# Optimization experiments

Hardware: AMD Instinct MI355X
Metric: run time of the kernel (lower is better)

The kernel has to match this reference:

```python
import jax, jax.numpy as jnp
from jax import lax
import numpy as np

NB = 4      # num_blocks
C = 1024    # model_channels
H = 16      # num_heads
P = 2       # patch_size
OUT_C = 64  # FinalLayer out_channels


def _sincos_1d(d, pos):
    omega = np.arange(d // 2, dtype=np.float64) / (d / 2.0)
    omega = 1.0 / 10000 ** omega
    out = np.einsum('m,d->md', pos.reshape(-1), omega)
    return np.concatenate([np.sin(out), np.cos(out)], axis=1)


def _sincos_2d(embed_dim, h, w):
    gh = np.arange(h, dtype=np.float32)
    gw = np.arange(w, dtype=np.float32)
    grid = np.stack(np.meshgrid(gw, gh), axis=0).reshape(2, 1, h, w)
    emb = np.concatenate([_sincos_1d(embed_dim // 2, grid[0]),
                          _sincos_1d(embed_dim // 2, grid[1])], axis=1)
    return jnp.asarray(emb, dtype=jnp.float32)  # (h*w, embed_dim)


def _ln(x, g, b, eps):
    mu = jnp.mean(x, axis=-1, keepdims=True)
    var = jnp.mean(jnp.square(x - mu), axis=-1, keepdims=True)
    y = (x - mu) * lax.rsqrt(var + eps)
    if g is not None:
        y = y * g + b
    return y


def _conv3x3(x, w, b):
    y = lax.conv_general_dilated(x, w, (1, 1), [(1, 1), (1, 1)],
                                 dimension_numbers=('NCHW', 'OIHW', 'NCHW'))
    return y + b[None, :, None, None]


def _forward(x, qkv_w, qkv_b, proj_w, proj_b, nq_g, nq_b, nk_g, nk_b,
             n1_g, n1_b, n2_g, n2_b, fc1_w, fc1_b, fc2_w, fc2_b,
             fin_w, fin_b, c1_w, c1_b, c2_w, c2_b):
    bs, l, c = x.shape
    h = w = int(np.sqrt(l))
    d = c // H
    scale = 1.0 / np.sqrt(d)
    x = x + _sincos_2d(c, h, w)[None]  # add 2D sincos pos embed
    for i in range(NB):
        # --- QK-norm attention ---
        res = x
        hn = _ln(x, n1_g[i], n1_b[i], 1e-5)
        qkv = hn @ qkv_w[i] + qkv_b[i]                 # (bs, l, 3c)
        q, k, v = jnp.split(qkv, 3, axis=-1)
        to_heads = lambda t: t.reshape(bs, l, H, d).transpose(0, 2, 1, 3)  # bhnd
        q = _ln(to_heads(q), nq_g[i], nq_b[i], 1e-5)
        k = _ln(to_heads(k), nk_g[i], nk_b[i], 1e-5)
        v = to_heads(v)
        attn = jax.nn.softmax(jnp.einsum('bhnd,bhmd->bhnm', q, k) * scale, axis=-1)
        o = jnp.einsum('bhnm,bhmd->bhnd', attn, v)
        o = o.transpose(0, 2, 1, 3).reshape(bs, l, c)
        x = res + (o @ proj_w[i] + proj_b[i])
        # --- MLP ---
        hn2 = _ln(x, n2_g[i], n2_b[i], 1e-5)
        mlp = jax.nn.gelu(hn2 @ fc1_w[i] + fc1_b[i], approximate=False) @ fc2_w[i] + fc2_b[i]
        x = x + mlp
    # --- final layer ---
    xf = _ln(x, None, None, 1e-6)
    xf = xf @ fin_w + fin_b                            # (bs, l, P*P*OUT_C)
    # --- unpatchify: last dim is flattened (c, p, p) ---
    xf = xf.reshape(bs, h, w, OUT_C, P, P)
    xf = jnp.einsum('bhwcpq->bhpwqc', xf).reshape(bs, h * P, w * P, OUT_C)
    xf = xf.transpose(0, 3, 1, 2)                      # (bs, 64, 64, 64)
    y = jax.nn.relu(_conv3x3(xf, c1_w, c1_b))
    y = _conv3x3(y, c2_w, c2_b)
    return y


def setup_inputs() -> dict:
    key = jax.random.key(0)
    ks = jax.random.split(key, 12)
    s = 0.02
    f = jnp.float32
    inp = {
        'x': jax.random.normal(ks[0], (2, 1024, C), f),
        'qkv_w': s * jax.random.normal(ks[1], (NB, C, 3 * C), f),
        'qkv_b': jnp.zeros((NB, 3 * C), f),
        'proj_w': s * jax.random.normal(ks[2], (NB, C, C), f),
        'proj_b': jnp.zeros((NB, C), f),
        'nq_g': jnp.ones((NB, C // H), f),
        'nq_b': jnp.zeros((NB, C // H), f),
        'nk_g': jnp.ones((NB, C // H), f),
        'nk_b': jnp.zeros((NB, C // H), f),
        'n1_g': jnp.ones((NB, C), f),
        'n1_b': jnp.zeros((NB, C), f),
        'n2_g': jnp.ones((NB, C), f),
        'n2_b': jnp.zeros((NB, C), f),
        'fc1_w': s * jax.random.normal(ks[3], (NB, C, 4 * C), f),
        'fc1_b': jnp.zeros((NB, 4 * C), f),
        'fc2_w': s * jax.random.normal(ks[4], (NB, 4 * C, C), f),
        'fc2_b': jnp.zeros((NB, C), f),
        'fin_w': s * jax.random.normal(ks[5], (C, P * P * OUT_C), f),
        'fin_b': jnp.zeros((P * P * OUT_C,), f),
        'c1_w': s * jax.random.normal(ks[6], (16, OUT_C, 3, 3), f),
        'c1_b': jnp.zeros((16,), f),
        'c2_w': s * jax.random.normal(ks[7], (3, 16, 3, 3), f),
        'c2_b': jnp.zeros((3,), f),
    }
    return inp


def reference(x, qkv_w, qkv_b, proj_w, proj_b, nq_g, nq_b, nk_g, nk_b,
              n1_g, n1_b, n2_g, n2_b, fc1_w, fc1_b, fc2_w, fc2_b,
              fin_w, fin_b, c1_w, c1_b, c2_w, c2_b):
    return _forward(x, qkv_w, qkv_b, proj_w, proj_b, nq_g, nq_b, nk_g, nk_b,
                    n1_g, n1_b, n2_g, n2_b, fc1_w, fc1_b, fc2_w, fc2_b,
                    fin_w, fin_b, c1_w, c1_b, c2_w, c2_b)
```

## Files before the change

### kernel.cpp

```cpp
#include <hip/hip_runtime.h>
#include <hip/hip_bf16.h>
#include <math.h>

typedef float floatx4 __attribute__((ext_vector_type(4)));
typedef short bf16x8 __attribute__((ext_vector_type(8)));

__device__ __forceinline__ unsigned short f2bf(float x) {
    union { float f; unsigned int u; } v; v.f = x;
    unsigned int r = v.u + 0x7fffu + ((v.u >> 16) & 1u);
    return (unsigned short)(r >> 16);
}

__device__ __forceinline__ void load_lds16(const void* g, void* l) {
    __builtin_amdgcn_global_load_lds(
        (const __attribute__((address_space(1))) unsigned int*)(uintptr_t)g,
        (__attribute__((address_space(3))) unsigned int*)(uintptr_t)l, 16, 0, 0);
}

__global__ void posembed_kernel(const float* __restrict__ xin, float* __restrict__ xb) {
    int idx = blockIdx.x * 256 + threadIdx.x;
    int c = idx & 1023;
    int n = (idx >> 10) & 1023;
    int pos = (c < 512) ? (n & 31) : (n >> 5);
    int cc = c & 511;
    int k = cc & 255;
    double om = exp(-(double)k * (9.210340371976184 / 256.0));
    double arg = (double)pos * om;
    float e = (float)((cc < 256) ? sin(arg) : cos(arg));
    xb[idx] = xin[idx] + e;
}

__global__ __launch_bounds__(256) void ln_kernel(const float* __restrict__ X,
                                                 unsigned short* __restrict__ Y,
                                                 const float* __restrict__ g,
                                                 const float* __restrict__ b,
                                                 float eps, int affine) {
    int row = blockIdx.x;
    const float4* xr = (const float4*)(X + (size_t)row * 1024);
    float4 x = xr[threadIdx.x];
    float s = x.x + x.y + x.z + x.w;
    float sq = x.x * x.x + x.y * x.y + x.z * x.z + x.w * x.w;
    __shared__ float red[8];
    #pragma unroll
    for (int off = 32; off; off >>= 1) { s += __shfl_xor(s, off); sq += __shfl_xor(sq, off); }
    int wid = threadIdx.x >> 6, lane = threadIdx.x & 63;
    if (!lane) { red[wid] = s; red[wid + 4] = sq; }
    __syncthreads();
    s = red[0] + red[1] + red[2] + red[3];
    sq = red[4] + red[5] + red[6] + red[7];
    float mu = s * (1.f / 1024.f);
    float var = sq * (1.f / 1024.f) - mu * mu;
    float rs = rsqrtf(var + eps);
    int c = threadIdx.x * 4;
    float4 y;
    if (affine) {
        y.x = (x.x - mu) * rs * g[c + 0] + b[c + 0];
        y.y = (x.y - mu) * rs * g[c + 1] + b[c + 1];
        y.z = (x.z - mu) * rs * g[c + 2] + b[c + 2];
        y.w = (x.w - mu) * rs * g[c + 3] + b[c + 3];
    } else {
        y.x = (x.x - mu) * rs; y.y = (x.y - mu) * rs;
        y.z = (x.z - mu) * rs; y.w = (x.w - mu) * rs;
    }
    ushort4 o;
    o.x = f2bf(y.x); o.y = f2bf(y.y); o.z = f2bf(y.z); o.w = f2bf(y.w);
    *(ushort4*)(Y + (size_t)row * 1024 + c) = o;
}

__global__ __launch_bounds__(256) void qkvprep_kernel(const float* __restrict__ qkv,
                                                      const float* __restrict__ nqg,
                                                      const float* __restrict__ nqb,
                                                      const float* __restrict__ nkg,
                                                      const float* __restrict__ nkb,
                                                      unsigned short* __restrict__ Qb,
                                                      unsigned short* __restrict__ Kb,
                                                      unsigned short* __restrict__ Vt) {
    __shared__ float t[64][65];
    int tid = threadIdx.x;
    int l0 = blockIdx.x * 64, h = blockIdx.y, b = blockIdx.z;
    for (int i = tid; i < 4096; i += 256) {
        int lr = i >> 6, dd = i & 63;
        t[lr][dd] = qkv[((size_t)(b * 1024 + l0 + lr)) * 3072 + 2048 + h * 64 + dd];
    }
    __syncthreads();
    for (int i = tid; i < 4096; i += 256) {
        int dd = i >> 6, lc = i & 63;
        Vt[((size_t)((b * 16 + h) * 64 + dd)) * 1024 + l0 + lc] = f2bf(t[lc][dd]);
    }
    int wave = tid >> 6, lane = tid & 63;
    float gq = nqg[lane], bq = nqb[lane], gk = nkg[lane], bk = nkb[lane];
    for (int i = 0; i < 16; i++) {
        int l = l0 + wave + 4 * i;
        const float* base = qkv + (size_t)(b * 1024 + l) * 3072 + h * 64 + lane;
        #pragma unroll
        for (int part = 0; part < 2; part++) {
            float v = base[part * 1024];
            float s = v, sq = v * v;
            #pragma unroll
            for (int off = 32; off; off >>= 1) { s += __shfl_xor(s, off); sq += __shfl_xor(sq, off); }
            float mu = s * (1.f / 64.f);
            float var = sq * (1.f / 64.f) - mu * mu;
            float rs = rsqrtf(var + 1e-5f);
            float y = (v - mu) * rs * (part ? gk : gq) + (part ? bk : bq);
            unsigned short* dst = part ? Kb : Qb;
            dst[(size_t)(b * 1024 + l) * 1024 + h * 64 + lane] = f2bf(y * (part ? 1.f : 0.125f));
        }
    }
}

__global__ __launch_bounds__(256) void attn_mfma(const unsigned short* __restrict__ Qb,
                                                 const unsigned short* __restrict__ Kb,
                                                 const unsigned short* __restrict__ Vt,
                                                 unsigned short* __restrict__ ob) {
    __shared__ short Ks[64 * 64];
    __shared__ short Vs[64 * 64];
    __shared__ short Pl[4][16 * 72];
    int tid = threadIdx.x;
    int lane = tid & 63, wave = tid >> 6;
    int ln16 = lane & 15, q = lane >> 4;
    int b = blockIdx.z, h = blockIdx.y, q0 = blockIdx.x * 64;
    int sw = ln16 & 7;
    int rc0 = (q ^ sw) * 8;
    int rc1 = ((4 + q) ^ sw) * 8;

    const unsigned short* qrow = Qb + ((size_t)(b * 1024 + q0 + wave * 16 + ln16)) * 1024 + h * 64;
    bf16x8 qf0 = *(const bf16x8*)(qrow + q * 8);
    bf16x8 qf1 = *(const bf16x8*)(qrow + 32 + q * 8);

    floatx4 o[4];
    #pragma unroll
    for (int td = 0; td < 4; td++) o[td] = (floatx4){0.f, 0.f, 0.f, 0.f};
    float mrow[4] = {-1e30f, -1e30f, -1e30f, -1e30f};
    float lrow[4] = {0.f, 0.f, 0.f, 0.f};

    const unsigned short* kbase0 = Kb + ((size_t)(b * 1024)) * 1024 + h * 64;
    const unsigned short* vbase0 = Vt + ((size_t)((b * 16 + h) * 64)) * 1024;

    for (int ch = 0; ch < 16; ch++) {
        int l0 = ch * 64;
        __syncthreads();
        #pragma unroll
        for (int it = 0; it < 2; it++) {
            int j = tid + it * 256;
            int row = j >> 3, g = j & 7, gc = g ^ (row & 7);
            load_lds16(kbase0 + (size_t)(l0 + row) * 1024 + gc * 8, &Ks[j * 8]);
            load_lds16(vbase0 + (size_t)row * 1024 + l0 + gc * 8, &Vs[j * 8]);
        }
        __syncthreads();

        floatx4 s[4];
        #pragma unroll
        for (int t = 0; t < 4; t++) {
            s[t] = (floatx4){0.f, 0.f, 0.f, 0.f};
            int kr = (t * 16 + ln16) * 64;
            bf16x8 kf0 = *(const bf16x8*)&Ks[kr + rc0];
            bf16x8 kf1 = *(const bf16x8*)&Ks[kr + rc1];
            s[t] = __builtin_amdgcn_mfma_f32_16x16x32_bf16(qf0, kf0, s[t], 0, 0, 0);
            s[t] = __builtin_amdgcn_mfma_f32_16x16x32_bf16(qf1, kf1, s[t], 0, 0, 0);
        }
        float cm[4], rs[4], p[4][4];
        #pragma unroll
        for (int r = 0; r < 4; r++)
            cm[r] = fmaxf(fmaxf(s[0][r], s[1][r]), fmaxf(s[2][r], s[3][r]));
        #pragma unroll
        for (int off = 1; off < 16; off <<= 1) {
            #pragma unroll
            for (int r = 0; r < 4; r++) cm[r] = fmaxf(cm[r], __shfl_xor(cm[r], off));
        }
        #pragma unroll
        for (int r = 0; r < 4; r++) {
            float mnew = fmaxf(mrow[r], cm[r]);
            float alpha = __expf(mrow[r] - mnew);
            mrow[r] = mnew;
            rs[r] = 0.f;
            #pragma unroll
            for (int t = 0; t < 4; t++) {
                p[t][r] = __expf(s[t][r] - mnew);
                rs[r] += p[t][r];
            }
            lrow[r] *= alpha;
            #pragma unroll
            for (int td = 0; td < 4; td++) o[td][r] *= alpha;
        }
        #pragma unroll
        for (int off = 1; off < 16; off <<= 1) {
            #pragma unroll
            for (int r = 0; r < 4; r++) rs[r] += __shfl_xor(rs[r], off);
        }
        #pragma unroll
        for (int r = 0; r < 4; r++) lrow[r] += rs[r];

        short* pw = &Pl[wave][0];
        #pragma unroll
        for (int t = 0; t < 4; t++)
            #pragma unroll
            for (int r = 0; r < 4; r++)
                pw[(q * 4 + r) * 72 + t * 16 + ln16] = (short)f2bf(p[t][r]);
        bf16x8 pf0 = *(const bf16x8*)&pw[ln16 * 72 + q * 8];
        bf16x8 pf1 = *(const bf16x8*)&pw[ln16 * 72 + 32 + q * 8];
        #pragma unroll
        for (int td = 0; td < 4; td++) {
            int vr = (td * 16 + ln16) * 64;
            bf16x8 vf0 = *(const bf16x8*)&Vs[vr + rc0];
            bf16x8 vf1 = *(const bf16x8*)&Vs[vr + rc1];
            o[td] = __builtin_amdgcn_mfma_f32_16x16x32_bf16(pf0, vf0, o[td], 0, 0, 0);
            o[td] = __builtin_amdgcn_mfma_f32_16x16x32_bf16(pf1, vf1, o[td], 0, 0, 0);
        }
    }
    #pragma unroll
    for (int td = 0; td < 4; td++) {
        #pragma unroll
        for (int r = 0; r < 4; r++) {
            int row = q0 + wave * 16 + q * 4 + r;
            int col = h * 64 + td * 16 + ln16;
            ob[((size_t)(b * 1024 + row)) * 1024 + col] = f2bf(o[td][r] / lrow[r]);
        }
    }
}

__global__ __launch_bounds__(256) void wtrans_kernel(const float* __restrict__ in,
                                                     unsigned short* __restrict__ out,
                                                     int K, int N) {
    __shared__ float t[64][65];
    int n0 = blockIdx.x * 64, k0 = blockIdx.y * 64, z = blockIdx.z;
    in  += (size_t)z * K * N;
    out += (size_t)z * N * K;
    for (int i = threadIdx.x; i < 4096; i += 256) {
        int kr = i >> 6, nc = i & 63;
        t[kr][nc] = in[(size_t)(k0 + kr) * N + n0 + nc];
    }
    __syncthreads();
    for (int i = threadIdx.x; i < 4096; i += 256) {
        int nr = i >> 6, kc = i & 63;
        out[(size_t)(n0 + nr) * K + k0 + kc] = f2bf(t[kc][nr]);
    }
}

template <int BM, int BN, int WM, int WN, int ACT, bool ADDC, bool OUTBF16, bool SPLITK>
__global__ __launch_bounds__(256) void gemm_bf16(const unsigned short* __restrict__ A,
                                                 const unsigned short* __restrict__ Bt,
                                                 const float* __restrict__ bias,
                                                 float* __restrict__ Cf,
                                                 unsigned short* __restrict__ Cb,
                                                 int M, int N, int K, int lda) {
    constexpr int MT = BM / (WM * 16);
    constexpr int NT = BN / (WN * 16);
    __shared__ short As[BM * 64];
    __shared__ short Bs[BN * 64];
    int tid = threadIdx.x;
    int lane = tid & 63, wave = tid >> 6;
    int wm = wave / WN, wn = wave % WN;
    int ln16 = lane & 15, q = lane >> 4;
    int m0 = blockIdx.y * BM, n0 = blockIdx.x * BN;
    int kOff = SPLITK ? blockIdx.z * K : 0;

    floatx4 acc[MT][NT];
    #pragma unroll
    for (int i = 0; i < MT; i++)
        #pragma unroll
        for (int j = 0; j < NT; j++) acc[i][j] = (floatx4){0.f, 0.f, 0.f, 0.f};

    int kSteps = K >> 6;
    for (int ks = 0; ks < kSteps; ks++) {
        int k0 = kOff + (ks << 6);
        #pragma unroll
        for (int it = 0; it < BM / 32; it++) {
            int i = tid + it * 256;
            int row = i >> 3, gc = (i & 7) ^ (row & 7);
            load_lds16(A + (size_t)(m0 + row) * lda + k0 + gc * 8, &As[i * 8]);
        }
        #pragma unroll
        for (int it = 0; it < BN / 32; it++) {
            int i = tid + it * 256;
            int row = i >> 3, gc = (i & 7) ^ (row & 7);
            load_lds16(Bt + (size_t)(n0 + row) * lda + k0 + gc * 8, &Bs[i * 8]);
        }
        __syncthreads();
        bf16x8 af[2][MT], bf[2][NT];
        #pragma unroll
        for (int h = 0; h < 2; h++) {
            #pragma unroll
            for (int mi = 0; mi < MT; mi++) {
                int row = wm * (BM / WM) + mi * 16 + ln16;
                af[h][mi] = *(const bf16x8*)&As[row * 64 + (((h * 4 + q) ^ (row & 7)) * 8)];
            }
            #pragma unroll
            for (int ni = 0; ni < NT; ni++) {
                int row = wn * (BN / WN) + ni * 16 + ln16;
                bf[h][ni] = *(const bf16x8*)&Bs[row * 64 + (((h * 4 + q) ^ (row & 7)) * 8)];
            }
        }
        #pragma unroll
        for (int h = 0; h < 2; h++)
            #pragma unroll
            for (int mi = 0; mi < MT; mi++)
                #pragma unroll
                for (int ni = 0; ni < NT; ni++)
                    acc[mi][ni] = __builtin_amdgcn_mfma_f32_16x16x32_bf16(af[h][mi], bf[h][ni], acc[mi][ni], 0, 0, 0);
        __syncthreads();
    }

    int q4 = q * 4;
    float* Cp = SPLITK ? (Cf + (size_t)blockIdx.z * M * N) : Cf;
    #pragma unroll
    for (int ni = 0; ni < NT; ni++) {
        int col = n0 + wn * (BN / WN) + ni * 16 + ln16;
        float bv = SPLITK ? 0.f : bias[col];
        #pragma unroll
        for (int mi = 0; mi < MT; mi++) {
            #pragma unroll
            for (int r = 0; r < 4; r++) {
                int row = m0 + wm * (BM / WM) + mi * 16 + q4 + r;
                size_t off = (size_t)row * N + col;
                float v = acc[mi][ni][r] + bv;
                if (!SPLITK && ACT == 1) v = 0.5f * v * (1.f + erff(v * 0.70710678118654752f));
                if (!SPLITK && ADDC) v += Cf[off];
                if (!SPLITK && OUTBF16) Cb[off] = f2bf(v);
                else Cp[off] = v;
            }
        }
    }
}

__global__ __launch_bounds__(256) void skreduce_kernel(const float* __restrict__ P,
                                                       const float* __restrict__ bias,
                                                       float* __restrict__ xb) {
    int idx = blockIdx.x * 256 + threadIdx.x;
    float4 a = ((const float4*)P)[idx];
    float4 b = ((const float4*)P)[idx + 524288];
    float4 x = ((float4*)xb)[idx];
    const float4 bb = *(const float4*)(bias + (idx & 255) * 4);
    x.x += a.x + b.x + bb.x;
    x.y += a.y + b.y + bb.y;
    x.z += a.z + b.z + bb.z;
    x.w += a.w + b.w + bb.w;
    ((float4*)xb)[idx] = x;
}

__global__ void unpatchify_kernel(const float* __restrict__ xf, float* __restrict__ img) {
    int idx = blockIdx.x * 256 + threadIdx.x;
    int x = idx & 63, y = (idx >> 6) & 63, ch = (idx >> 12) & 63, b = idx >> 18;
    int hh = y >> 1, ww = x >> 1, p = y & 1, qq = x & 1;
    img[idx] = xf[((size_t)b * 1024 + hh * 32 + ww) * 256 + ch * 4 + p * 2 + qq];
}

__global__ __launch_bounds__(256) void conv1_kernel(const float* __restrict__ img,
                                                    const float* __restrict__ w,
                                                    const float* __restrict__ bias,
                                                    float* __restrict__ out) {
    __shared__ float Ls[64 * 3 * 66];
    __shared__ float Ws[16 * 580];
    int tid = threadIdx.x;
    int y = blockIdx.x, b = blockIdx.y;
    for (int i = tid; i < 9216; i += 256) {
        int oc = i / 576, rem = i % 576;
        Ws[oc * 580 + rem] = w[i];
    }
    for (int i = tid; i < 12288; i += 256) {
        int r = i >> 6, x = i & 63;
        int ic = r / 3, ky = r % 3;
        int yy = y + ky - 1;
        float v = (yy >= 0 && yy < 64) ? img[((size_t)(b * 64 + ic) * 64 + yy) * 64 + x] : 0.f;
        Ls[(ic * 3 + ky) * 66 + x + 1] = v;
        if (x == 0)  Ls[(ic * 3 + ky) * 66 + 0]  = 0.f;
        if (x == 63) Ls[(ic * 3 + ky) * 66 + 65] = 0.f;
    }
    __syncthreads();
    int oc = tid >> 4, xg = (tid & 15) * 4;
    float bv = bias[oc];
    float acc0 = bv, acc1 = bv, acc2 = bv, acc3 = bv;
    for (int ic = 0; ic < 64; ic++) {
        const float* wr = &Ws[oc * 580 + ic * 9];
        float w00 = wr[0], w01 = wr[1], w02 = wr[2];
        float w10 = wr[3], w11 = wr[4], w12 = wr[5];
        float w20 = wr[6], w21 = wr[7], w22 = wr[8];
        const float* l0 = &Ls[(ic * 3 + 0) * 66 + xg];
        const float* l1 = &Ls[(ic * 3 + 1) * 66 + xg];
        const float* l2 = &Ls[(ic * 3 + 2) * 66 + xg];
        float a0 = l0[0], a1 = l0[1], a2 = l0[2], a3 = l0[3], a4 = l0[4], a5 = l0[5];
        float b0 = l1[0], b1 = l1[1], b2 = l1[2], b3 = l1[3], b4 = l1[4], b5 = l1[5];
        float c0 = l2[0], c1 = l2[1], c2 = l2[2], c3 = l2[3], c4 = l2[4], c5 = l2[5];
        acc0 += a0*w00 + a1*w01 + a2*w02 + b0*w10 + b1*w11 + b2*w12 + c0*w20 + c1*w21 + c2*w22;
        acc1 += a1*w00 + a2*w01 + a3*w02 + b1*w10 + b2*w11 + b3*w12 + c1*w20 + c2*w21 + c3*w22;
        acc2 += a2*w00 + a3*w01 + a4*w02 + b2*w10 + b3*w11 + b4*w12 + c2*w20 + c3*w21 + c4*w22;
        acc3 += a3*w00 + a4*w01 + a5*w02 + b3*w10 + b4*w11 + b5*w12 + c3*w20 + c4*w21 + c5*w22;
    }
    float* op = out + (((size_t)(b * 16 + oc) * 64 + y) * 64 + xg);
    op[0] = fmaxf(acc0, 0.f);
    op[1] = fmaxf(acc1, 0.f);
    op[2] = fmaxf(acc2, 0.f);
    op[3] = fmaxf(acc3, 0.f);
}

__global__ __launch_bounds__(256) void conv2_kernel(const float* __restrict__ in,
                                                    const float* __restrict__ w,
                                                    const float* __restrict__ bias,
                                                    float* __restrict__ out) {
    __shared__ float Ls[16 * 3 * 66];
    __shared__ float Ws[3 * 160];
    int tid = threadIdx.x;
    int y = blockIdx.x, b = blockIdx.y;
    for (int i = tid; i < 432; i += 256) {
        int oc = i / 144, rem = i % 144;
        Ws[oc * 160 + rem] = w[i];
    }
    for (int i = tid; i < 3072; i += 256) {
        int r = i >> 6, x = i & 63;
        int ic = r / 3, ky = r % 3;
        int yy = y + ky - 1;
        float v = (yy >= 0 && yy < 64) ? in[((size_t)(b * 16 + ic) * 64 + yy) * 64 + x] : 0.f;
        Ls[(ic * 3 + ky) * 66 + x + 1] = v;
        if (x == 0)  Ls[(ic * 3 + ky) * 66 + 0]  = 0.f;
        if (x == 63) Ls[(ic * 3 + ky) * 66 + 65] = 0.f;
    }
    __syncthreads();
    int oc = tid >> 6, x = tid & 63;
    if (oc < 3) {
        float acc = bias[oc];
        for (int ic = 0; ic < 16; ic++) {
            const float* wr = &Ws[oc * 160 + ic * 9];
            const float* l0 = &Ls[(ic * 3 + 0) * 66 + x];
            const float* l1 = &Ls[(ic * 3 + 1) * 66 + x];
            const float* l2 = &Ls[(ic * 3 + 2) * 66 + x];
            acc += l0[0]*wr[0] + l0[1]*wr[1] + l0[2]*wr[2]
                 + l1[0]*wr[3] + l1[1]*wr[4] + l1[2]*wr[5]
                 + l2[0]*wr[6] + l2[1]*wr[7] + l2[2]*wr[8];
        }
        out[((size_t)(b * 3 + oc) * 64 + y) * 64 + x] = acc;
    }
}

extern "C" void kernel_launch(void* const* d_in, const int* in_sizes, int n_in,
                              void* d_out, int out_size, void* d_ws, size_t ws_size,
                              hipStream_t stream) {
    const float* x_in   = (const float*)d_in[0];
    const float* qkv_w  = (const float*)d_in[1];
    const float* qkv_b  = (const float*)d_in[2];
    const float* proj_w = (const float*)d_in[3];
    const float* proj_b = (const float*)d_in[4];
    const float* nq_g   = (const float*)d_in[5];
    const float* nq_b   = (const float*)d_in[6];
    const float* nk_g   = (const float*)d_in[7];
    const float* nk_b   = (const float*)d_in[8];
    const float* n1_g   = (const float*)d_in[9];
    const float* n1_b   = (const float*)d_in[10];
    const float* n2_g   = (const float*)d_in[11];
    const float* n2_b   = (const float*)d_in[12];
    const float* fc1_w  = (const float*)d_in[13];
    const float* fc1_b  = (const float*)d_in[14];
    const float* fc2_w  = (const float*)d_in[15];
    const float* fc2_b  = (const float*)d_in[16];
    const float* fin_w  = (const float*)d_in[17];
    const float* fin_b  = (const float*)d_in[18];
    const float* c1_w   = (const float*)d_in[19];
    const float* c1_b   = (const float*)d_in[20];
    const float* c2_w   = (const float*)d_in[21];
    const float* c2_b   = (const float*)d_in[22];
    float* out = (float*)d_out;

    char* w = (char*)d_ws;
    float* xb           = (float*)w;          w += (size_t)2 * 1024 * 1024 * 4;
    unsigned short* hnb = (unsigned short*)w; w += (size_t)2 * 1024 * 1024 * 2;
    float* qkv          = (float*)w;          w += (size_t)2 * 1024 * 3072 * 4;
    unsigned short* obb = (unsigned short*)w; w += (size_t)2 * 1024 * 1024 * 2;
    unsigned short* mhb = (unsigned short*)w; w += (size_t)2 * 1024 * 4096 * 2;
    float* xf           = (float*)w;          w += (size_t)2 * 1024 * 256 * 4;
    float* img          = (float*)w;          w += (size_t)2 * 64 * 64 * 64 * 4;
    float* c1o          = (float*)w;          w += (size_t)2 * 16 * 64 * 64 * 4;
    unsigned short* Qb  = (unsigned short*)w; w += (size_t)2 * 1024 * 1024 * 2;
    unsigned short* Kb  = (unsigned short*)w; w += (size_t)2 * 1024 * 1024 * 2;
    unsigned short* Vt  = (unsigned short*)w; w += (size_t)2 * 16 * 64 * 1024 * 2;
    float* skb          = (float*)w;          w += (size_t)2 * 2048 * 1024 * 4;
    unsigned short* WQ  = (unsigned short*)w; w += (size_t)4 * 1024 * 3072 * 2;
    unsigned short* WP  = (unsigned short*)w; w += (size_t)4 * 1024 * 1024 * 2;
    unsigned short* W1  = (unsigned short*)w; w += (size_t)4 * 1024 * 4096 * 2;
    unsigned short* W2  = (unsigned short*)w; w += (size_t)4 * 4096 * 1024 * 2;
    unsigned short* WF  = (unsigned short*)w; w += (size_t)1024 * 256 * 2;

    wtrans_kernel<<<dim3(48, 16, 4), 256, 0, stream>>>(qkv_w, WQ, 1024, 3072);
    wtrans_kernel<<<dim3(16, 16, 4), 256, 0, stream>>>(proj_w, WP, 1024, 1024);
    wtrans_kernel<<<dim3(64, 16, 4), 256, 0, stream>>>(fc1_w, W1, 1024, 4096);
    wtrans_kernel<<<dim3(16, 64, 4), 256, 0, stream>>>(fc2_w, W2, 4096, 1024);
    wtrans_kernel<<<dim3(4, 16, 1), 256, 0, stream>>>(fin_w, WF, 1024, 256);

    posembed_kernel<<<8192, 256, 0, stream>>>(x_in, xb);

    for (int i = 0; i < 4; i++) {
        ln_kernel<<<2048, 256, 0, stream>>>(xb, hnb, n1_g + i * 1024, n1_b + i * 1024, 1e-5f, 1);
        gemm_bf16<64, 128, 2, 2, 0, false, false, false><<<dim3(24, 32), 256, 0, stream>>>(
            hnb, WQ + (size_t)i * 3072 * 1024, qkv_b + i * 3072, qkv, nullptr, 2048, 3072, 1024, 1024);
        qkvprep_kernel<<<dim3(16, 16, 2), 256, 0, stream>>>(
            qkv, nq_g + i * 64, nq_b + i * 64, nk_g + i * 64, nk_b + i * 64, Qb, Kb, Vt);
        attn_mfma<<<dim3(16, 16, 2), 256, 0, stream>>>(Qb, Kb, Vt, obb);
        gemm_bf16<64, 64, 2, 2, 0, true, false, false><<<dim3(16, 32), 256, 0, stream>>>(
            obb, WP + (size_t)i * 1024 * 1024, proj_b + i * 1024, xb, nullptr, 2048, 1024, 1024, 1024);
        ln_kernel<<<2048, 256, 0, stream>>>(xb, hnb, n2_g + i * 1024, n2_b + i * 1024, 1e-5f, 1);
        gemm_bf16<64, 128, 2, 2, 1, false, true, false><<<dim3(32, 32), 256, 0, stream>>>(
            hnb, W1 + (size_t)i * 4096 * 1024, fc1_b + i * 4096, nullptr, mhb, 2048, 4096, 1024, 1024);
        gemm_bf16<64, 64, 2, 2, 0, false, false, true><<<dim3(16, 32, 2), 256, 0, stream>>>(
            mhb, W2 + (size_t)i * 1024 * 4096, fc2_b + i * 1024, skb, nullptr, 2048, 1024, 2048, 4096);
        skreduce_kernel<<<2048, 256, 0, stream>>>(skb, fc2_b + i * 1024, xb);
    }

    ln_kernel<<<2048, 256, 0, stream>>>(xb, hnb, nullptr, nullptr, 1e-6f, 0);
    gemm_bf16<64, 64, 2, 2, 0, false, false, false><<<dim3(4, 32), 256, 0, stream>>>(
        hnb, WF, fin_b, xf, nullptr, 2048, 256, 1024, 1024);
    unpatchify_kernel<<<2048, 256, 0, stream>>>(xf, img);
    conv1_kernel<<<dim3(64, 2), 256, 0, stream>>>(img, c1_w, c1_b, c1o);
    conv2_kernel<<<dim3(64, 2), 256, 0, stream>>>(c1o, c2_w, c2_b, out);
}
```

Before: 1.016 ms.

## Double-buffer K/V tiles in attention and use float math for pos embed

The attention kernel now keeps two LDS buffers for K and V and prefetches the next 64-row chunk while the current one is computed. Partial vmcnt waits and raw barriers replace the two __syncthreads per chunk, so global-to-LDS loads overlap with MFMA work. The positional-embedding kernel also switches from double-precision exp/sin/cos to single-precision versions. This cuts slow FP64 math at some cost in accuracy for larger arguments. The double buffer doubles K/V LDS use, which may lower occupancy.

Result: faster. 986.0 us (-3.0%).

```diff
diff --git a/kernel.cpp b/kernel.cpp
--- a/kernel.cpp
+++ b/kernel.cpp
@@ -24,9 +24,9 @@
     int pos = (c < 512) ? (n & 31) : (n >> 5);
     int cc = c & 511;
     int k = cc & 255;
-    double om = exp(-(double)k * (9.210340371976184 / 256.0));
-    double arg = (double)pos * om;
-    float e = (float)((cc < 256) ? sin(arg) : cos(arg));
+    float om = expf(-(float)k * (9.210340371976184f / 256.0f));
+    float arg = (float)pos * om;
+    float e = (cc < 256) ? sinf(arg) : cosf(arg);
     xb[idx] = xin[idx] + e;
 }
 
@@ -112,8 +112,8 @@
                                                  const unsigned short* __restrict__ Kb,
                                                  const unsigned short* __restrict__ Vt,
                                                  unsigned short* __restrict__ ob) {
-    __shared__ short Ks[64 * 64];
-    __shared__ short Vs[64 * 64];
+    __shared__ short Ks[2][64 * 64];
+    __shared__ short Vs[2][64 * 64];
     __shared__ short Pl[4][16 * 72];
     int tid = threadIdx.x;
     int lane = tid & 63, wave = tid >> 6;
@@ -136,25 +136,36 @@
     const unsigned short* kbase0 = Kb + ((size_t)(b * 1024)) * 1024 + h * 64;
     const unsigned short* vbase0 = Vt + ((size_t)((b * 16 + h) * 64)) * 1024;
 
-    for (int ch = 0; ch < 16; ch++) {
-        int l0 = ch * 64;
-        __syncthreads();
+    auto stage = [&](int bi, int l0) {
         #pragma unroll
         for (int it = 0; it < 2; it++) {
             int j = tid + it * 256;
             int row = j >> 3, g = j & 7, gc = g ^ (row & 7);
-            load_lds16(kbase0 + (size_t)(l0 + row) * 1024 + gc * 8, &Ks[j * 8]);
-            load_lds16(vbase0 + (size_t)row * 1024 + l0 + gc * 8, &Vs[j * 8]);
-        }
-        __syncthreads();
+            load_lds16(kbase0 + (size_t)(l0 + row) * 1024 + gc * 8, &Ks[bi][j * 8]);
+            load_lds16(vbase0 + (size_t)row * 1024 + l0 + gc * 8, &Vs[bi][j * 8]);
+        }
+    };
+
+    stage(0, 0);
+    for (int ch = 0; ch < 16; ch++) {
+        int cur = ch & 1;
+        __builtin_amdgcn_s_barrier();
+        if (ch < 15) {
+            stage(cur ^ 1, (ch + 1) * 64);
+            asm volatile("s_waitcnt vmcnt(4)" ::: "memory");
+        } else {
+            asm volatile("s_waitcnt vmcnt(0)" ::: "memory");
+        }
+        __builtin_amdgcn_s_barrier();
+        __builtin_amdgcn_sched_barrier(0);
 
         floatx4 s[4];
         #pragma unroll
         for (int t = 0; t < 4; t++) {
             s[t] = (floatx4){0.f, 0.f, 0.f, 0.f};
             int kr = (t * 16 + ln16) * 64;
-            bf16x8 kf0 = *(const bf16x8*)&Ks[kr + rc0];
-            bf16x8 kf1 = *(const bf16x8*)&Ks[kr + rc1];
+            bf16x8 kf0 = *(const bf16x8*)&Ks[cur][kr + rc0];
+            bf16x8 kf1 = *(const bf16x8*)&Ks[cur][kr + rc1];
             s[t] = __builtin_amdgcn_mfma_f32_16x16x32_bf16(qf0, kf0, s[t], 0, 0, 0);
             s[t] = __builtin_amdgcn_mfma_f32_16x16x32_bf16(qf1, kf1, s[t], 0, 0, 0);
         }
@@ -201,8 +212,8 @@
         #pragma unroll
         for (int td = 0; td < 4; td++) {
             int vr = (td * 16 + ln16) * 64;
-            bf16x8 vf0 = *(const bf16x8*)&Vs[vr + rc0];
-            bf16x8 vf1 = *(const bf16x8*)&Vs[vr + rc1];
+            bf16x8 vf0 = *(const bf16x8*)&Vs[cur][vr + rc0];
+            bf16x8 vf1 = *(const bf16x8*)&Vs[cur][vr + rc1];
             o[td] = __builtin_amdgcn_mfma_f32_16x16x32_bf16(pf0, vf0, o[td], 0, 0, 0);
             o[td] = __builtin_amdgcn_mfma_f32_16x16x32_bf16(pf1, vf1, o[td], 0, 0, 0);
         }
```
